# Kernel optimization log

Hardware: AMD Instinct MI355X
Metric: run time of the kernel (lower is better)

The kernel has to match this reference:

```python
import jax, jax.numpy as jnp
import numpy as np

B, N, F, H, M, EF, OUT = 256, 32, 40, 100, 100, 4, 128
MESSAGE_PASSES = 3


def setup_inputs() -> dict:
    key = jax.random.key(0)
    ks = jax.random.split(key, 8)
    # Deterministic ring graphs: node i <-> node (i+1)%N, one-hot bond type.
    # Every node has degree 2 -> static nonzero counts.
    rng = np.random.default_rng(0)
    edges = np.zeros((B, N, N, EF), np.float32)
    b = np.arange(B)[:, None]
    i = np.arange(N)[None, :]
    j = (i + 1) % N
    t = rng.integers(0, EF, size=(B, N))
    edges[b, i, j, t] = 1.0
    edges[b, j, i, t] = 1.0

    nodes = jax.random.normal(ks[0], (B, N, F), jnp.float32)

    def init(k, shape, fan):
        return jax.random.normal(k, shape, jnp.float32) / np.sqrt(fan).astype(np.float32)

    W_msg = init(ks[1], (M, H, EF), H)          # MNN edge-conditioned weights
    W_ih = init(ks[2], (3 * H, M), M)            # GRUCell input weights
    W_hh = init(ks[3], (3 * H, H), H)            # GRUCell hidden weights
    b_ih = jnp.zeros((3 * H,), jnp.float32)
    b_hh = jnp.zeros((3 * H,), jnp.float32)
    Wg = init(ks[4], (H + F, H), H + F)          # gather gate
    bg = jnp.zeros((H,), jnp.float32)
    We = init(ks[5], (H, H), H)                  # gather embed
    be = jnp.zeros((H,), jnp.float32)
    Wo = init(ks[6], (H, OUT), H)                # output head
    bo = jnp.zeros((OUT,), jnp.float32)

    return {
        "nodes": nodes, "edges": jnp.asarray(edges),
        "W_msg": W_msg, "W_ih": W_ih, "W_hh": W_hh, "b_ih": b_ih, "b_hh": b_hh,
        "Wg": Wg, "bg": bg, "We": We, "be": be, "Wo": Wo, "bo": bo,
        "n_edges": B * N * 2, "n_node_entries": B * N,
    }


def gru_cell(x, h, W_ih, W_hh, b_ih, b_hh):
    gi = x @ W_ih.T + b_ih
    gh = h @ W_hh.T + b_hh
    ir, iz, inn = jnp.split(gi, 3, axis=-1)
    hr, hz, hn = jnp.split(gh, 3, axis=-1)
    r = jax.nn.sigmoid(ir + hr)
    z = jax.nn.sigmoid(iz + hz)
    n = jnp.tanh(inn + r * hn)
    return (1.0 - z) * n + z * h


def reference(nodes, edges, W_msg, W_ih, W_hh, b_ih, b_hh, Wg, bg, We, be, Wo, bo,
              n_edges, n_node_entries):
    adjacency = jnp.sum(edges, axis=3)                      # (B, N, N)
    eb, en, eg = jnp.nonzero(adjacency, size=n_edges)       # edge-level indices
    nb, nn_ = jnp.nonzero(adjacency.sum(-1), size=n_node_entries)

    # Dense one-hot segment-sum matrix: (n_node_entries, n_edges)
    same = (nb[:, None] == eb) & (nn_[:, None] == en)
    msg_sum_mat = same.astype(jnp.float32)

    edge_batch_edges = edges[eb, en, eg, :]                 # (E, EF)

    hidden = jnp.zeros((B, N, H), jnp.float32).at[:, :, :F].set(nodes)
    node_h = hidden[nb, nn_, :]                             # (V, H)

    for _ in range(MESSAGE_PASSES):
        nghb_h = hidden[eb, eg, :]                          # (E, H)
        # MNN message: sum_f edges[e,f] * W_msg[m,h,f] * nghb[e,h]
        message_terms = jnp.einsum('ef,mhf,eh->em', edge_batch_edges, W_msg, nghb_h)
        messages = msg_sum_mat @ message_terms              # (V, M) dense one-hot matmul
        node_h = gru_cell(messages, node_h, W_ih, W_hh, b_ih, b_hh)
        hidden = hidden.at[nb, nn_, :].set(node_h)

    node_mask = (adjacency.sum(-1) != 0).astype(jnp.float32)  # (B, N)
    cat = jnp.concatenate([hidden, nodes], axis=-1)           # (B, N, H+F)
    gate = jax.nn.sigmoid(cat @ Wg + bg)
    emb = gate * (hidden @ We + be)
    graph_emb = jnp.sum(emb * node_mask[..., None], axis=1)   # (B, H)
    return graph_emb @ Wo + bo                                # (B, OUT)
```

## Files before the change

kernel.cpp:

```cpp
#include <hip/hip_runtime.h>
#include <cstddef>
#include <cstdint>

#define B_   256
#define N_   32
#define F_   40
#define H_   100
#define OUT_ 128
#define TB   512
#define XCS  168
#define XMS  136
#define AWS  40
#define ZSP  40
#define NBLK 343
#define NLO  63

using bf16x8 = __attribute__((ext_vector_type(8))) short;
using f32x4  = __attribute__((ext_vector_type(4))) float;

#define MFMA(a,b,c) __builtin_amdgcn_mfma_f32_16x16x32_bf16((a),(b),(c),0,0,0)

__device__ __forceinline__ float sigmoidf_(float x){ return 1.0f/(1.0f+__expf(-x)); }
__device__ __forceinline__ float tanhf_(float x){
  float e = __expf(2.0f*x);
  return 1.0f - 2.0f/(e+1.0f);
}
__device__ __forceinline__ float bf2f(short s){ return __uint_as_float(((uint32_t)(uint16_t)s)<<16); }
__device__ __forceinline__ short f2bf(float x){
  uint32_t u = __float_as_uint(x);
  return (short)((u + 0x7FFFu + ((u>>16)&1u))>>16);
}
__device__ __forceinline__ void bsplit(float x, short& hi, short& lo){
  hi = f2bf(x);
  lo = f2bf(x - bf2f(hi));
}

__global__ void prep_frags4(const float* __restrict__ Wmsg,
                            const float* __restrict__ Wih,
                            const float* __restrict__ Whh,
                            const float* __restrict__ Wg,
                            const float* __restrict__ We,
                            short* __restrict__ AFhi,
                            short* __restrict__ AFlo){
  int slot = blockIdx.x*blockDim.x + threadIdx.x;
  if (slot >= NBLK*512) return;
  int blk = slot>>9, r = slot&511, lane = r>>3, jj = r&7;
  int m = lane&15, q = lane>>4, kl = q*8+jj;
  float v = 0.0f;
  if (blk < 112){
    int t = blk/28, rem = blk%28, jmt = rem>>2, ks = rem&3;
    int mg = jmt*16+m, h = ks*32+kl;
    if (mg<100 && h<100) v = Wmsg[(mg*100+h)*4 + t];
    AFhi[slot] = f2bf(v);
  } else if (blk < 280){
    int bb = blk-112, mat = bb/28, rem = bb%28, jmt = rem>>2, ks = rem&3;
    int mg = jmt*16+m, k = ks*32+kl;
    if (mg<100 && k<100)
      v = (mat<3) ? Wih[(mat*100+mg)*100+k] : Whh[((mat-3)*100+mg)*100+k];
    AFhi[slot] = f2bf(v);
  } else if (blk < 315){
    int bb = blk-280, jmt = bb/5, ks = bb%5;
    int mg = jmt*16+m, k = ks*32+kl;
    if (mg<100 && k<140) v = Wg[k*100+mg];
    short hi,lo; bsplit(v,hi,lo);
    AFhi[slot] = hi;
    AFlo[(size_t)(blk-280)*512 + r] = lo;
  } else {
    int bb = blk-315, jmt = bb>>2, ks = bb&3;
    int mg = jmt*16+m, k = ks*32+kl;
    if (mg<100 && k<100) v = We[k*100+mg];
    short hi,lo; bsplit(v,hi,lo);
    AFhi[slot] = hi;
    AFlo[(size_t)(blk-280)*512 + r] = lo;
  }
}

__global__ __launch_bounds__(TB, 2) void mpnn_mfma(
    const float* __restrict__ nodes, const float* __restrict__ edges,
    const short* __restrict__ AFhi, const short* __restrict__ AFlo,
    const float* __restrict__ b_ih, const float* __restrict__ b_hh,
    const float* __restrict__ bg, const float* __restrict__ be,
    const float* __restrict__ Wo, const float* __restrict__ bo,
    float* __restrict__ out){
  const int b = blockIdx.x;
  const int tid = threadIdx.x;
  const int lane = tid & 63;
  const int w = tid >> 6;

  __shared__ short XcH[32*XCS];
  __shared__ short XmH[32*XMS];
  __shared__ short Aw[4][32*AWS];
  __shared__ short Zs[7*4*16*ZSP];
  __shared__ float sh_ge[H_];
  __shared__ float sh_part[4][OUT_];
  __shared__ int   sh_msk[N_];

  for (int i=tid;i<(32*XCS)/2;i+=TB){ ((int*)XcH)[i]=0; }
  for (int i=tid;i<(32*XMS)/2;i+=TB){ ((int*)XmH)[i]=0; }
  if (tid < H_) sh_ge[tid]=0.0f;
  __syncthreads();

  for (int e=tid; e<N_*N_; e+=TB){
    int n = e>>5, g = e&31;
    const float4 ev = *(const float4*)(edges + (((size_t)b*N_+n)*N_+g)*4);
    float adj = ev.x+ev.y+ev.z+ev.w;
    unsigned long long bal = __ballot(adj != 0.0f);
    if (lane == 0)  sh_msk[n] = ((int)(bal & 0xFFFFFFFFull)) != 0;
    if (lane == 32) sh_msk[n] = ((int)(bal >> 32)) != 0;
    Aw[0][n*AWS+g] = f2bf(ev.x);
    Aw[1][n*AWS+g] = f2bf(ev.y);
    Aw[2][n*AWS+g] = f2bf(ev.z);
    Aw[3][n*AWS+g] = f2bf(ev.w);
  }
  for (int p=tid; p<N_*F_; p+=TB){
    int n = p/F_, f = p%F_;
    float x = nodes[((size_t)b*N_+n)*F_ + f];
    short hi = f2bf(x);
    XcH[n*XCS+f]=hi;
    XcH[n*XCS+100+f]=hi;
  }

  const int jmt = w;
  const bool task = (w < 7);
  const int c16 = lane & 15;
  const int q   = lane >> 4;
  const int boff = q*8;
  const int rowbase = jmt*16 + q*4;
  const int n0 = c16, n1 = 16 + c16;

  bf16x8 Ai[3][4], Ah[3][4];
  if (task){
#pragma unroll
    for (int mat=0; mat<3; ++mat){
#pragma unroll
      for (int ks=0; ks<4; ++ks){
        Ai[mat][ks] = *(const bf16x8*)(AFhi + ((size_t)(112 + mat*28 + jmt*4 + ks))*512 + lane*8);
        Ah[mat][ks] = *(const bf16x8*)(AFhi + ((size_t)(112 + (3+mat)*28 + jmt*4 + ks))*512 + lane*8);
      }
    }
  }
  float bi0[4],bi1[4],bi2[4],bh0[4],bh1[4],bh2[4];
  if (task){
#pragma unroll
    for (int r=0;r<4;++r){
      int row = rowbase + r;
      bool ok = row < 100;
      bi0[r] = ok ? b_ih[row]       : 0.0f;
      bi1[r] = ok ? b_ih[100+row]   : 0.0f;
      bi2[r] = ok ? b_ih[200+row]   : 0.0f;
      bh0[r] = ok ? b_hh[row]       : 0.0f;
      bh1[r] = ok ? b_hh[100+row]   : 0.0f;
      bh2[r] = ok ? b_hh[200+row]   : 0.0f;
    }
  }

  float hst0[4]={0.f,0.f,0.f,0.f}, hst1[4]={0.f,0.f,0.f,0.f};
  if (task){
#pragma unroll
    for (int r=0;r<4;++r){
      int row = rowbase + r;
      if (row < F_){
        hst0[r] = nodes[((size_t)b*N_+n0)*F_ + row];
        hst1[r] = nodes[((size_t)b*N_+n1)*F_ + row];
      }
    }
  }
  __syncthreads();

  for (int pass=0; pass<3; ++pass){
    f32x4 Chh[3][2];
#pragma unroll
    for (int m3=0;m3<3;++m3){ Chh[m3][0]=(f32x4)0.0f; Chh[m3][1]=(f32x4)0.0f; }
    if (task){
      const short* pb0 = XcH + n0*XCS + boff;
      const short* pb1 = XcH + n1*XCS + boff;
      bf16x8 x0[4], x1[4];
#pragma unroll
      for (int ks=0;ks<4;++ks){
        x0[ks] = *(const bf16x8*)(pb0 + ks*32);
        x1[ks] = *(const bf16x8*)(pb1 + ks*32);
      }
      f32x4 Cm0=(f32x4)0.0f, Cm1=(f32x4)0.0f;
#pragma unroll
      for (int th=0; th<2; ++th){
        f32x4 Za[2][2];
#pragma unroll
        for (int u=0;u<2;++u){
          int t = th*2+u;
          const short* pa = AFhi + ((size_t)(t*28 + jmt*4))*512 + lane*8;
          bf16x8 a0 = *(const bf16x8*)(pa);
          bf16x8 a1 = *(const bf16x8*)(pa+512);
          bf16x8 a2 = *(const bf16x8*)(pa+1024);
          bf16x8 a3 = *(const bf16x8*)(pa+1536);
          Za[u][0]=(f32x4)0.0f; Za[u][1]=(f32x4)0.0f;
          Za[u][0]=MFMA(a0,x0[0],Za[u][0]); Za[u][0]=MFMA(a1,x0[1],Za[u][0]);
          Za[u][0]=MFMA(a2,x0[2],Za[u][0]); Za[u][0]=MFMA(a3,x0[3],Za[u][0]);
          Za[u][1]=MFMA(a0,x1[0],Za[u][1]); Za[u][1]=MFMA(a1,x1[1],Za[u][1]);
          Za[u][1]=MFMA(a2,x1[2],Za[u][1]); Za[u][1]=MFMA(a3,x1[3],Za[u][1]);
        }
#pragma unroll
        for (int u=0;u<2;++u){
          int t = th*2+u;
          int zb = (w*4+t)*16*ZSP;
#pragma unroll
          for (int r=0;r<4;++r){
            Zs[zb + (q*4+r)*ZSP + c16]      = f2bf(Za[u][0][r]);
            Zs[zb + (q*4+r)*ZSP + c16 + 16] = f2bf(Za[u][1][r]);
          }
        }
#pragma unroll
        for (int u=0;u<2;++u){
          int t = th*2+u;
          int zb = (w*4+t)*16*ZSP;
          bf16x8 az  = *(const bf16x8*)&Zs[zb + c16*ZSP + boff];
          bf16x8 bt0 = *(const bf16x8*)&Aw[t][n0*AWS + boff];
          bf16x8 bt1 = *(const bf16x8*)&Aw[t][n1*AWS + boff];
          Cm0 = MFMA(az, bt0, Cm0);
          Cm1 = MFMA(az, bt1, Cm1);
        }
      }
      if (rowbase < 100){
        short4 pk0, pk1;
        pk0.x=f2bf(Cm0[0]); pk0.y=f2bf(Cm0[1]); pk0.z=f2bf(Cm0[2]); pk0.w=f2bf(Cm0[3]);
        pk1.x=f2bf(Cm1[0]); pk1.y=f2bf(Cm1[1]); pk1.z=f2bf(Cm1[2]); pk1.w=f2bf(Cm1[3]);
        *(short4*)&XmH[n0*XMS + rowbase] = pk0;
        *(short4*)&XmH[n1*XMS + rowbase] = pk1;
      }
#pragma unroll
      for (int m3=0;m3<3;++m3){
#pragma unroll
        for (int ks=0;ks<4;++ks){
          Chh[m3][0] = MFMA(Ah[m3][ks], x0[ks], Chh[m3][0]);
          Chh[m3][1] = MFMA(Ah[m3][ks], x1[ks], Chh[m3][1]);
        }
      }
    }
    __syncthreads();
    if (task){
      const short* pm0 = XmH + n0*XMS + boff;
      const short* pm1 = XmH + n1*XMS + boff;
      bf16x8 m0f[4], m1f[4];
#pragma unroll
      for (int ks=0;ks<4;++ks){
        m0f[ks] = *(const bf16x8*)(pm0 + ks*32);
        m1f[ks] = *(const bf16x8*)(pm1 + ks*32);
      }
      f32x4 Ci[3][2];
#pragma unroll
      for (int m3=0;m3<3;++m3){ Ci[m3][0]=(f32x4)0.0f; Ci[m3][1]=(f32x4)0.0f; }
#pragma unroll
      for (int m3=0;m3<3;++m3){
#pragma unroll
        for (int ks=0;ks<4;++ks){
          Ci[m3][0] = MFMA(Ai[m3][ks], m0f[ks], Ci[m3][0]);
          Ci[m3][1] = MFMA(Ai[m3][ks], m1f[ks], Ci[m3][1]);
        }
      }
      if (rowbase < 100){
        bool k0 = sh_msk[n0] != 0, k1 = sh_msk[n1] != 0;
        short4 pk0, pk1;
#pragma unroll
        for (int r=0;r<4;++r){
          {
            float ho = hst0[r];
            float rr = sigmoidf_(Ci[0][0][r]+Chh[0][0][r] + bi0[r] + bh0[r]);
            float zz = sigmoidf_(Ci[1][0][r]+Chh[1][0][r] + bi1[r] + bh1[r]);
            float nn = tanhf_(Ci[2][0][r] + bi2[r] + rr*(Chh[2][0][r] + bh2[r]));
            float hnew = (1.0f-zz)*nn + zz*ho;
            if (!k0) hnew = ho;
            hst0[r] = hnew;
            ((short*)&pk0)[r] = f2bf(hnew);
          }
          {
            float ho = hst1[r];
            float rr = sigmoidf_(Ci[0][1][r]+Chh[0][1][r] + bi0[r] + bh0[r]);
            float zz = sigmoidf_(Ci[1][1][r]+Chh[1][1][r] + bi1[r] + bh1[r]);
            float nn = tanhf_(Ci[2][1][r] + bi2[r] + rr*(Chh[2][1][r] + bh2[r]));
            float hnew = (1.0f-zz)*nn + zz*ho;
            if (!k1) hnew = ho;
            hst1[r] = hnew;
            ((short*)&pk1)[r] = f2bf(hnew);
          }
        }
        *(short4*)&XcH[n0*XCS + rowbase] = pk0;
        *(short4*)&XcH[n1*XCS + rowbase] = pk1;
      }
    }
    __syncthreads();
  }

  if (task){
    const short* pb0 = XcH + n0*XCS + boff;
    const short* pb1 = XcH + n1*XCS + boff;
    bf16x8 rb0[5], rb1[5];
#pragma unroll
    for (int ks=0;ks<5;++ks){
      rb0[ks] = *(const bf16x8*)(pb0 + ks*32);
      rb1[ks] = *(const bf16x8*)(pb1 + ks*32);
    }
    f32x4 Cg0=(f32x4)0.0f, Cg1=(f32x4)0.0f, Ce0=(f32x4)0.0f, Ce1=(f32x4)0.0f;
    {
      const short* ph = AFhi + ((size_t)(280 + jmt*5))*512 + lane*8;
      const short* pl = AFlo + ((size_t)(jmt*5))*512 + lane*8;
#pragma unroll
      for (int ks=0;ks<5;++ks){
        bf16x8 ah = *(const bf16x8*)(ph + ks*512);
        bf16x8 al = *(const bf16x8*)(pl + ks*512);
        Cg0 = MFMA(ah, rb0[ks], Cg0); Cg0 = MFMA(al, rb0[ks], Cg0);
        Cg1 = MFMA(ah, rb1[ks], Cg1); Cg1 = MFMA(al, rb1[ks], Cg1);
      }
    }
    {
      const short* ph = AFhi + ((size_t)(315 + jmt*4))*512 + lane*8;
      const short* pl = AFlo + ((size_t)(35 + jmt*4))*512 + lane*8;
#pragma unroll
      for (int ks=0;ks<4;++ks){
        bf16x8 ah = *(const bf16x8*)(ph + ks*512);
        bf16x8 al = *(const bf16x8*)(pl + ks*512);
        Ce0 = MFMA(ah, rb0[ks], Ce0); Ce0 = MFMA(al, rb0[ks], Ce0);
        Ce1 = MFMA(ah, rb1[ks], Ce1); Ce1 = MFMA(al, rb1[ks], Ce1);
      }
    }
    bool k0 = sh_msk[n0] != 0, k1 = sh_msk[n1] != 0;
#pragma unroll
    for (int r=0;r<4;++r){
      int row = rowbase + r;
      float v0 = 0.0f, v1 = 0.0f;
      if (row<100){
        float g0 = sigmoidf_(Cg0[r] + bg[row]);
        float g1 = sigmoidf_(Cg1[r] + bg[row]);
        float e0 = g0*(Ce0[r] + be[row]);
        float e1 = g1*(Ce1[r] + be[row]);
        v0 = k0 ? e0 : 0.0f;
        v1 = k1 ? e1 : 0.0f;
      }
      float v = v0 + v1;
      v += __shfl_xor(v, 1);
      v += __shfl_xor(v, 2);
      v += __shfl_xor(v, 4);
      v += __shfl_xor(v, 8);
      if (row<100 && (lane&15)==0) atomicAdd(&sh_ge[row], v);
    }
  }
  __syncthreads();
  {
    int o = tid & 127, qq = tid >> 7;
    float s = 0.0f;
    int k0 = 25*qq;
#pragma unroll 5
    for (int k=k0; k<k0+25; ++k) s += sh_ge[k]*Wo[k*OUT_+o];
    sh_part[qq][o] = s;
  }
  __syncthreads();
  if (tid < OUT_){
    out[(size_t)b*OUT_ + tid] = bo[tid] + sh_part[0][tid] + sh_part[1][tid]
                              + sh_part[2][tid] + sh_part[3][tid];
  }
}

extern "C" void kernel_launch(void* const* d_in, const int* in_sizes, int n_in,
                              void* d_out, int out_size, void* d_ws, size_t ws_size,
                              hipStream_t stream){
  const float* nodes = (const float*)d_in[0];
  const float* edges = (const float*)d_in[1];
  const float* W_msg = (const float*)d_in[2];
  const float* W_ih  = (const float*)d_in[3];
  const float* W_hh  = (const float*)d_in[4];
  const float* b_ih  = (const float*)d_in[5];
  const float* b_hh  = (const float*)d_in[6];
  const float* Wg    = (const float*)d_in[7];
  const float* bg    = (const float*)d_in[8];
  const float* We    = (const float*)d_in[9];
  const float* be    = (const float*)d_in[10];
  const float* Wo    = (const float*)d_in[11];
  const float* bo    = (const float*)d_in[12];

  short* AFhi = (short*)d_ws;
  short* AFlo = AFhi + (size_t)NBLK*512;

  prep_frags4<<<(NBLK*512 + 255)/256, 256, 0, stream>>>(W_msg, W_ih, W_hh, Wg, We,
                                                        AFhi, AFlo);
  mpnn_mfma<<<B_, TB, 0, stream>>>(nodes, edges, AFhi, AFlo, b_ih, b_hh, bg, be,
                                   Wo, bo, (float*)d_out);
}
```

Baseline: 108.9 us.

## Fuse weight fragment prep into main kernel and merge GRU accumulators

Removes the separate prep kernel that converted weights to bf16 MFMA fragments. Each block now loads and converts W_msg, W_ih and W_hh into registers directly, and converts Wg/We on the fly in the gather stage. This saves a launch and a global round trip. The GRU input and hidden products for the r/z gates now share accumulators with pre-summed biases, and the W_hh MFMAs are interleaved with the B-operand loads. The cost is redundant, strided scalar global loads and conversions in all 256 blocks, plus more registers (Am is held in registers), which may reduce occupancy or cause spills.

```diff
diff --git a/kernel.cpp b/kernel.cpp
--- a/kernel.cpp
+++ b/kernel.cpp
@@ -12,8 +12,6 @@
 #define XMS  136
 #define AWS  40
 #define ZSP  40
-#define NBLK 343
-#define NLO  63
 
 using bf16x8 = __attribute__((ext_vector_type(8))) short;
 using f32x4  = __attribute__((ext_vector_type(4))) float;
@@ -30,56 +28,14 @@
   uint32_t u = __float_as_uint(x);
   return (short)((u + 0x7FFFu + ((u>>16)&1u))>>16);
 }
-__device__ __forceinline__ void bsplit(float x, short& hi, short& lo){
-  hi = f2bf(x);
-  lo = f2bf(x - bf2f(hi));
-}
-
-__global__ void prep_frags4(const float* __restrict__ Wmsg,
-                            const float* __restrict__ Wih,
-                            const float* __restrict__ Whh,
-                            const float* __restrict__ Wg,
-                            const float* __restrict__ We,
-                            short* __restrict__ AFhi,
-                            short* __restrict__ AFlo){
-  int slot = blockIdx.x*blockDim.x + threadIdx.x;
-  if (slot >= NBLK*512) return;
-  int blk = slot>>9, r = slot&511, lane = r>>3, jj = r&7;
-  int m = lane&15, q = lane>>4, kl = q*8+jj;
-  float v = 0.0f;
-  if (blk < 112){
-    int t = blk/28, rem = blk%28, jmt = rem>>2, ks = rem&3;
-    int mg = jmt*16+m, h = ks*32+kl;
-    if (mg<100 && h<100) v = Wmsg[(mg*100+h)*4 + t];
-    AFhi[slot] = f2bf(v);
-  } else if (blk < 280){
-    int bb = blk-112, mat = bb/28, rem = bb%28, jmt = rem>>2, ks = rem&3;
-    int mg = jmt*16+m, k = ks*32+kl;
-    if (mg<100 && k<100)
-      v = (mat<3) ? Wih[(mat*100+mg)*100+k] : Whh[((mat-3)*100+mg)*100+k];
-    AFhi[slot] = f2bf(v);
-  } else if (blk < 315){
-    int bb = blk-280, jmt = bb/5, ks = bb%5;
-    int mg = jmt*16+m, k = ks*32+kl;
-    if (mg<100 && k<140) v = Wg[k*100+mg];
-    short hi,lo; bsplit(v,hi,lo);
-    AFhi[slot] = hi;
-    AFlo[(size_t)(blk-280)*512 + r] = lo;
-  } else {
-    int bb = blk-315, jmt = bb>>2, ks = bb&3;
-    int mg = jmt*16+m, k = ks*32+kl;
-    if (mg<100 && k<100) v = We[k*100+mg];
-    short hi,lo; bsplit(v,hi,lo);
-    AFhi[slot] = hi;
-    AFlo[(size_t)(blk-280)*512 + r] = lo;
-  }
-}
-
-__global__ __launch_bounds__(TB, 2) void mpnn_mfma(
+
+__global__ __launch_bounds__(TB, 2) void mpnn_fused(
     const float* __restrict__ nodes, const float* __restrict__ edges,
-    const short* __restrict__ AFhi, const short* __restrict__ AFlo,
+    const float* __restrict__ Wmsg, const float* __restrict__ Wih,
+    const float* __restrict__ Whh,
     const float* __restrict__ b_ih, const float* __restrict__ b_hh,
-    const float* __restrict__ bg, const float* __restrict__ be,
+    const float* __restrict__ Wg, const float* __restrict__ bg,
+    const float* __restrict__ We, const float* __restrict__ be,
     const float* __restrict__ Wo, const float* __restrict__ bo,
     float* __restrict__ out){
   const int b = blockIdx.x;
@@ -128,37 +84,57 @@
   const int rowbase = jmt*16 + q*4;
   const int n0 = c16, n1 = 16 + c16;
 
-  bf16x8 Ai[3][4], Ah[3][4];
+  bf16x8 Am[4][4], Ai[3][4], Ah[3][4];
+  float bs0[4],bs1[4],bi2[4],bh2[4];
+  float hst0[4]={0.f,0.f,0.f,0.f}, hst1[4]={0.f,0.f,0.f,0.f};
   if (task){
-#pragma unroll
-    for (int mat=0; mat<3; ++mat){
-#pragma unroll
-      for (int ks=0; ks<4; ++ks){
-        Ai[mat][ks] = *(const bf16x8*)(AFhi + ((size_t)(112 + mat*28 + jmt*4 + ks))*512 + lane*8);
-        Ah[mat][ks] = *(const bf16x8*)(AFhi + ((size_t)(112 + (3+mat)*28 + jmt*4 + ks))*512 + lane*8);
-      }
-    }
-  }
-  float bi0[4],bi1[4],bi2[4],bh0[4],bh1[4],bh2[4];
-  if (task){
+    const int mg = jmt*16 + c16;
+    const bool mok = (mg < 100);
+#pragma unroll
+    for (int t=0;t<4;++t){
+#pragma unroll
+      for (int ks=0;ks<4;++ks){
+        bf16x8 f;
+#pragma unroll
+        for (int jj=0;jj<8;++jj){
+          int h = ks*32 + q*8 + jj;
+          float v = (mok && h<100) ? Wmsg[((size_t)(mg*100+h))*4 + t] : 0.0f;
+          f[jj] = f2bf(v);
+        }
+        Am[t][ks] = f;
+      }
+    }
+#pragma unroll
+    for (int mat=0;mat<3;++mat){
+      const size_t roff = (size_t)(mat*100 + (mok ? mg : 0))*100;
+#pragma unroll
+      for (int ks=0;ks<4;++ks){
+        bf16x8 fi, fh;
+#pragma unroll
+        for (int jj=0;jj<8;++jj){
+          int k = ks*32 + q*8 + jj;
+          bool ok = mok && (k < 100);
+          float vi = ok ? Wih[roff + k] : 0.0f;
+          float vh = ok ? Whh[roff + k] : 0.0f;
+          fi[jj] = f2bf(vi);
+          fh[jj] = f2bf(vh);
+        }
+        Ai[mat][ks] = fi;
+        Ah[mat][ks] = fh;
+      }
+    }
 #pragma unroll
     for (int r=0;r<4;++r){
       int row = rowbase + r;
       bool ok = row < 100;
-      bi0[r] = ok ? b_ih[row]       : 0.0f;
-      bi1[r] = ok ? b_ih[100+row]   : 0.0f;
-      bi2[r] = ok ? b_ih[200+row]   : 0.0f;
-      bh0[r] = ok ? b_hh[row]       : 0.0f;
-      bh1[r] = ok ? b_hh[100+row]   : 0.0f;
-      bh2[r] = ok ? b_hh[200+row]   : 0.0f;
-    }
-  }
-
-  float hst0[4]={0.f,0.f,0.f,0.f}, hst1[4]={0.f,0.f,0.f,0.f};
-  if (task){
-#pragma unroll
-    for (int r=0;r<4;++r){
-      int row = rowbase + r;
+      float a0 = ok ? b_ih[row]     : 0.0f;
+      float a1 = ok ? b_hh[row]     : 0.0f;
+      float a2 = ok ? b_ih[100+row] : 0.0f;
+      float a3 = ok ? b_hh[100+row] : 0.0f;
+      bs0[r] = a0 + a1;
+      bs1[r] = a2 + a3;
+      bi2[r] = ok ? b_ih[200+row] : 0.0f;
+      bh2[r] = ok ? b_hh[200+row] : 0.0f;
       if (row < F_){
         hst0[r] = nodes[((size_t)b*N_+n0)*F_ + row];
         hst1[r] = nodes[((size_t)b*N_+n1)*F_ + row];
@@ -172,52 +148,38 @@
 #pragma unroll
     for (int m3=0;m3<3;++m3){ Chh[m3][0]=(f32x4)0.0f; Chh[m3][1]=(f32x4)0.0f; }
     if (task){
-      const short* pb0 = XcH + n0*XCS + boff;
-      const short* pb1 = XcH + n1*XCS + boff;
-      bf16x8 x0[4], x1[4];
 #pragma unroll
       for (int ks=0;ks<4;++ks){
-        x0[ks] = *(const bf16x8*)(pb0 + ks*32);
-        x1[ks] = *(const bf16x8*)(pb1 + ks*32);
+        bf16x8 x0 = *(const bf16x8*)&XcH[n0*XCS + ks*32 + boff];
+        bf16x8 x1 = *(const bf16x8*)&XcH[n1*XCS + ks*32 + boff];
+#pragma unroll
+        for (int m3=0;m3<3;++m3){
+          Chh[m3][0] = MFMA(Ah[m3][ks], x0, Chh[m3][0]);
+          Chh[m3][1] = MFMA(Ah[m3][ks], x1, Chh[m3][1]);
+        }
       }
       f32x4 Cm0=(f32x4)0.0f, Cm1=(f32x4)0.0f;
 #pragma unroll
-      for (int th=0; th<2; ++th){
-        f32x4 Za[2][2];
-#pragma unroll
-        for (int u=0;u<2;++u){
-          int t = th*2+u;
-          const short* pa = AFhi + ((size_t)(t*28 + jmt*4))*512 + lane*8;
-          bf16x8 a0 = *(const bf16x8*)(pa);
-          bf16x8 a1 = *(const bf16x8*)(pa+512);
-          bf16x8 a2 = *(const bf16x8*)(pa+1024);
-          bf16x8 a3 = *(const bf16x8*)(pa+1536);
-          Za[u][0]=(f32x4)0.0f; Za[u][1]=(f32x4)0.0f;
-          Za[u][0]=MFMA(a0,x0[0],Za[u][0]); Za[u][0]=MFMA(a1,x0[1],Za[u][0]);
-          Za[u][0]=MFMA(a2,x0[2],Za[u][0]); Za[u][0]=MFMA(a3,x0[3],Za[u][0]);
-          Za[u][1]=MFMA(a0,x1[0],Za[u][1]); Za[u][1]=MFMA(a1,x1[1],Za[u][1]);
-          Za[u][1]=MFMA(a2,x1[2],Za[u][1]); Za[u][1]=MFMA(a3,x1[3],Za[u][1]);
-        }
-#pragma unroll
-        for (int u=0;u<2;++u){
-          int t = th*2+u;
-          int zb = (w*4+t)*16*ZSP;
-#pragma unroll
-          for (int r=0;r<4;++r){
-            Zs[zb + (q*4+r)*ZSP + c16]      = f2bf(Za[u][0][r]);
-            Zs[zb + (q*4+r)*ZSP + c16 + 16] = f2bf(Za[u][1][r]);
-          }
-        }
-#pragma unroll
-        for (int u=0;u<2;++u){
-          int t = th*2+u;
-          int zb = (w*4+t)*16*ZSP;
-          bf16x8 az  = *(const bf16x8*)&Zs[zb + c16*ZSP + boff];
-          bf16x8 bt0 = *(const bf16x8*)&Aw[t][n0*AWS + boff];
-          bf16x8 bt1 = *(const bf16x8*)&Aw[t][n1*AWS + boff];
-          Cm0 = MFMA(az, bt0, Cm0);
-          Cm1 = MFMA(az, bt1, Cm1);
-        }
+      for (int t=0;t<4;++t){
+        f32x4 Za0=(f32x4)0.0f, Za1=(f32x4)0.0f;
+#pragma unroll
+        for (int ks=0;ks<4;++ks){
+          bf16x8 g0 = *(const bf16x8*)&XcH[c16*XCS      + ks*32 + boff];
+          bf16x8 g1 = *(const bf16x8*)&XcH[(16+c16)*XCS + ks*32 + boff];
+          Za0 = MFMA(Am[t][ks], g0, Za0);
+          Za1 = MFMA(Am[t][ks], g1, Za1);
+        }
+        int zb = (w*4+t)*16*ZSP;
+#pragma unroll
+        for (int r=0;r<4;++r){
+          Zs[zb + (q*4+r)*ZSP + c16]      = f2bf(Za0[r]);
+          Zs[zb + (q*4+r)*ZSP + c16 + 16] = f2bf(Za1[r]);
+        }
+        bf16x8 az  = *(const bf16x8*)&Zs[zb + c16*ZSP + boff];
+        bf16x8 bt0 = *(const bf16x8*)&Aw[t][n0*AWS + boff];
+        bf16x8 bt1 = *(const bf16x8*)&Aw[t][n1*AWS + boff];
+        Cm0 = MFMA(az, bt0, Cm0);
+        Cm1 = MFMA(az, bt1, Cm1);
       }
       if (rowbase < 100){
         short4 pk0, pk1;
@@ -226,35 +188,20 @@
         *(short4*)&XmH[n0*XMS + rowbase] = pk0;
         *(short4*)&XmH[n1*XMS + rowbase] = pk1;
       }
-#pragma unroll
-      for (int m3=0;m3<3;++m3){
-#pragma unroll
-        for (int ks=0;ks<4;++ks){
-          Chh[m3][0] = MFMA(Ah[m3][ks], x0[ks], Chh[m3][0]);
-          Chh[m3][1] = MFMA(Ah[m3][ks], x1[ks], Chh[m3][1]);
-        }
-      }
     }
     __syncthreads();
     if (task){
-      const short* pm0 = XmH + n0*XMS + boff;
-      const short* pm1 = XmH + n1*XMS + boff;
-      bf16x8 m0f[4], m1f[4];
+      f32x4 Ci2a=(f32x4)0.0f, Ci2b=(f32x4)0.0f;
 #pragma unroll
       for (int ks=0;ks<4;++ks){
-        m0f[ks] = *(const bf16x8*)(pm0 + ks*32);
-        m1f[ks] = *(const bf16x8*)(pm1 + ks*32);
-      }
-      f32x4 Ci[3][2];
-#pragma unroll
-      for (int m3=0;m3<3;++m3){ Ci[m3][0]=(f32x4)0.0f; Ci[m3][1]=(f32x4)0.0f; }
-#pragma unroll
-      for (int m3=0;m3<3;++m3){
-#pragma unroll
-        for (int ks=0;ks<4;++ks){
-          Ci[m3][0] = MFMA(Ai[m3][ks], m0f[ks], Ci[m3][0]);
-          Ci[m3][1] = MFMA(Ai[m3][ks], m1f[ks], Ci[m3][1]);
-        }
+        bf16x8 m0 = *(const bf16x8*)&XmH[n0*XMS + ks*32 + boff];
+        bf16x8 m1 = *(const bf16x8*)&XmH[n1*XMS + ks*32 + boff];
+        Chh[0][0] = MFMA(Ai[0][ks], m0, Chh[0][0]);
+        Chh[0][1] = MFMA(Ai[0][ks], m1, Chh[0][1]);
+        Chh[1][0] = MFMA(Ai[1][ks], m0, Chh[1][0]);
+        Chh[1][1] = MFMA(Ai[1][ks], m1, Chh[1][1]);
+        Ci2a      = MFMA(Ai[2][ks], m0, Ci2a);
+        Ci2b      = MFMA(Ai[2][ks], m1, Ci2b);
       }
       if (rowbase < 100){
         bool k0 = sh_msk[n0] != 0, k1 = sh_msk[n1] != 0;
@@ -263,9 +210,9 @@
         for (int r=0;r<4;++r){
           {
             float ho = hst0[r];
-            float rr = sigmoidf_(Ci[0][0][r]+Chh[0][0][r] + bi0[r] + bh0[r]);
-            float zz = sigmoidf_(Ci[1][0][r]+Chh[1][0][r] + bi1[r] + bh1[r]);
-            float nn = tanhf_(Ci[2][0][r] + bi2[r] + rr*(Chh[2][0][r] + bh2[r]));
+            float rr = sigmoidf_(Chh[0][0][r] + bs0[r]);
+            float zz = sigmoidf_(Chh[1][0][r] + bs1[r]);
+            float nn = tanhf_(Ci2a[r] + bi2[r] + rr*(Chh[2][0][r] + bh2[r]));
             float hnew = (1.0f-zz)*nn + zz*ho;
             if (!k0) hnew = ho;
             hst0[r] = hnew;
@@ -273,9 +220,9 @@
           }
           {
             float ho = hst1[r];
-            float rr = sigmoidf_(Ci[0][1][r]+Chh[0][1][r] + bi0[r] + bh0[r]);
-            float zz = sigmoidf_(Ci[1][1][r]+Chh[1][1][r] + bi1[r] + bh1[r]);
-            float nn = tanhf_(Ci[2][1][r] + bi2[r] + rr*(Chh[2][1][r] + bh2[r]));
+            float rr = sigmoidf_(Chh[0][1][r] + bs0[r]);
+            float zz = sigmoidf_(Chh[1][1][r] + bs1[r]);
+            float nn = tanhf_(Ci2b[r] + bi2[r] + rr*(Chh[2][1][r] + bh2[r]));
             float hnew = (1.0f-zz)*nn + zz*ho;
             if (!k1) hnew = ho;
             hst1[r] = hnew;
@@ -290,36 +237,40 @@
   }
 
   if (task){
-    const short* pb0 = XcH + n0*XCS + boff;
-    const short* pb1 = XcH + n1*XCS + boff;
-    bf16x8 rb0[5], rb1[5];
+    const int jg = jmt*16 + c16;
+    const bool jok = jg < 100;
+    f32x4 Cg0=(f32x4)0.0f, Cg1=(f32x4)0.0f, Ce0=(f32x4)0.0f, Ce1=(f32x4)0.0f;
 #pragma unroll
     for (int ks=0;ks<5;++ks){
-      rb0[ks] = *(const bf16x8*)(pb0 + ks*32);
-      rb1[ks] = *(const bf16x8*)(pb1 + ks*32);
-    }
-    f32x4 Cg0=(f32x4)0.0f, Cg1=(f32x4)0.0f, Ce0=(f32x4)0.0f, Ce1=(f32x4)0.0f;
-    {
-      const short* ph = AFhi + ((size_t)(280 + jmt*5))*512 + lane*8;
-      const short* pl = AFlo + ((size_t)(jmt*5))*512 + lane*8;
-#pragma unroll
-      for (int ks=0;ks<5;++ks){
-        bf16x8 ah = *(const bf16x8*)(ph + ks*512);
-        bf16x8 al = *(const bf16x8*)(pl + ks*512);
-        Cg0 = MFMA(ah, rb0[ks], Cg0); Cg0 = MFMA(al, rb0[ks], Cg0);
-        Cg1 = MFMA(ah, rb1[ks], Cg1); Cg1 = MFMA(al, rb1[ks], Cg1);
-      }
-    }
-    {
-      const short* ph = AFhi + ((size_t)(315 + jmt*4))*512 + lane*8;
-      const short* pl = AFlo + ((size_t)(35 + jmt*4))*512 + lane*8;
-#pragma unroll
-      for (int ks=0;ks<4;++ks){
-        bf16x8 ah = *(const bf16x8*)(ph + ks*512);
-        bf16x8 al = *(const bf16x8*)(pl + ks*512);
-        Ce0 = MFMA(ah, rb0[ks], Ce0); Ce0 = MFMA(al, rb0[ks], Ce0);
-        Ce1 = MFMA(ah, rb1[ks], Ce1); Ce1 = MFMA(al, rb1[ks], Ce1);
-      }
+      bf16x8 gh, gl;
+#pragma unroll
+      for (int jj=0;jj<8;++jj){
+        int k = ks*32 + q*8 + jj;
+        float v = (jok && k<140) ? Wg[(size_t)k*100 + jg] : 0.0f;
+        short hi = f2bf(v);
+        short lo = f2bf(v - bf2f(hi));
+        gh[jj]=hi; gl[jj]=lo;
+      }
+      bf16x8 r0 = *(const bf16x8*)&XcH[n0*XCS + ks*32 + boff];
+      bf16x8 r1 = *(const bf16x8*)&XcH[n1*XCS + ks*32 + boff];
+      Cg0 = MFMA(gh, r0, Cg0); Cg0 = MFMA(gl, r0, Cg0);
+      Cg1 = MFMA(gh, r1, Cg1); Cg1 = MFMA(gl, r1, Cg1);
+    }
+#pragma unroll
+    for (int ks=0;ks<4;++ks){
+      bf16x8 eh, el;
+#pragma unroll
+      for (int jj=0;jj<8;++jj){
+        int k = ks*32 + q*8 + jj;
+        float v = (jok && k<100) ? We[(size_t)k*100 + jg] : 0.0f;
+        short hi = f2bf(v);
+        short lo = f2bf(v - bf2f(hi));
+        eh[jj]=hi; el[jj]=lo;
+      }
+      bf16x8 r0 = *(const bf16x8*)&XcH[n0*XCS + ks*32 + boff];
+      bf16x8 r1 = *(const bf16x8*)&XcH[n1*XCS + ks*32 + boff];
+      Ce0 = MFMA(eh, r0, Ce0); Ce0 = MFMA(el, r0, Ce0);
+      Ce1 = MFMA(eh, r1, Ce1); Ce1 = MFMA(el, r1, Ce1);
     }
     bool k0 = sh_msk[n0] != 0, k1 = sh_msk[n1] != 0;
 #pragma unroll
@@ -374,12 +325,9 @@
   const float* be    = (const float*)d_in[10];
   const float* Wo    = (const float*)d_in[11];
   const float* bo    = (const float*)d_in[12];
-
-  short* AFhi = (short*)d_ws;
-  short* AFlo = AFhi + (size_t)NBLK*512;
-
-  prep_frags4<<<(NBLK*512 + 255)/256, 256, 0, stream>>>(W_msg, W_ih, W_hh, Wg, We,
-                                                        AFhi, AFlo);
-  mpnn_mfma<<<B_, TB, 0, stream>>>(nodes, edges, AFhi, AFlo, b_ih, b_hh, bg, be,
-                                   Wo, bo, (float*)d_out);
+  (void)d_ws; (void)ws_size;
+
+  mpnn_fused<<<B_, TB, 0, stream>>>(nodes, edges, W_msg, W_ih, W_hh,
+                                    b_ih, b_hh, Wg, bg, We, be, Wo, bo,
+                                    (float*)d_out);
 }
```

Result: slower. 195.3 us (+79.3%).
